# Performance work log

Measured on AMD Instinct MI355X. Metric: run time of the kernel, lower is better.

Reference implementation:

```python
import jax, jax.numpy as jnp
import numpy as np

NUM_HEADS = 8
DIM_HEAD = 64
GROUPS = 32
EPS = 1e-5


def setup_inputs() -> dict:
    key = jax.random.key(0)
    k1, k2, k3 = jax.random.split(key, 3)
    C = 512
    inner = NUM_HEADS * DIM_HEAD  # 512
    x = jax.random.normal(k1, (8, C, 32, 32), dtype=jnp.float32)
    gamma = jnp.ones((C,), dtype=jnp.float32)
    beta = jnp.zeros((C,), dtype=jnp.float32)
    w_qkv = jax.random.normal(k2, (3 * inner, C), dtype=jnp.float32) * 0.02
    w_out = jax.random.normal(k3, (C, inner), dtype=jnp.float32) * 0.02
    return {"x": x, "gamma": gamma, "beta": beta, "w_qkv": w_qkv, "w_out": w_out}


def group_norm(x, gamma, beta):
    b, c, h, w = x.shape
    xg = x.reshape(b, GROUPS, c // GROUPS, h, w)
    mean = jnp.mean(xg, axis=(2, 3, 4), keepdims=True)
    var = jnp.var(xg, axis=(2, 3, 4), keepdims=True)
    xn = ((xg - mean) * jax.lax.rsqrt(var + EPS)).reshape(b, c, h, w)
    return xn * gamma[None, :, None, None] + beta[None, :, None, None]


def reference(x, gamma, beta, w_qkv, w_out):
    b, c, h, w = x.shape
    H, d = NUM_HEADS, DIM_HEAD
    inner = H * d
    scale = d ** (-0.5)
    residual = x
    xn = group_norm(x, gamma, beta)
    # 1x1 conv (no bias) == channel matmul
    qkv = jnp.einsum('bchw,oc->bohw', xn, w_qkv)  # [b, 3*inner, h, w]
    q, k, v = jnp.split(qkv, 3, axis=1)
    def to_heads(t):
        # b (H d) h w -> b H (h w) d
        return t.reshape(b, H, d, h * w).transpose(0, 1, 3, 2)
    q, k, v = to_heads(q), to_heads(k), to_heads(v)
    attn = jnp.einsum('bhid,bhjd->bhij', q, k) * scale  # [b,H,hw,hw]
    attn = jax.nn.softmax(attn, axis=-1)
    out = jnp.einsum('bhij,bhjd->bhid', attn, v)  # [b,H,hw,d]
    # b H (h w) d -> b (H d) h w
    out = out.transpose(0, 1, 3, 2).reshape(b, inner, h, w)
    out = jnp.einsum('bchw,oc->bohw', out, w_out)
    return out + residual
```

## Files before the change

kernel.cpp:

```cpp
#include <hip/hip_runtime.h>


typedef __attribute__((ext_vector_type(8))) short bf16x8;
typedef __attribute__((ext_vector_type(4))) short bf16x4;
typedef __attribute__((ext_vector_type(4))) float f32x4;

#define NB 8
#define NC 512
#define HW 1024
#define NHEAD 8
#define DHEAD 64
#define GROUPS 32
#define CPG 16
#define QKV_N 1536

#define GLL16(gaddr, ldsaddr)                                                  \
    __builtin_amdgcn_global_load_lds(                                          \
        (const __attribute__((address_space(1))) unsigned*)(gaddr),            \
        (__attribute__((address_space(3))) unsigned*)(ldsaddr), 16, 0, 0)

__device__ alignas(64) short g_xn[(size_t)8192 * 512];
__device__ alignas(64) short g_qkv[(size_t)8192 * 1536];
__device__ alignas(64) short g_vt[(size_t)64 * 64 * 1024];
__device__ alignas(64) short g_attno[(size_t)8192 * 512];
__device__ alignas(64) short g_wqkv[(size_t)1536 * 512];
__device__ alignas(64) short g_wout[(size_t)512 * 512];

__device__ __forceinline__ float b2f(short h) {
    union { unsigned u; float f; } v;
    v.u = ((unsigned)(unsigned short)h) << 16;
    return v.f;
}
__device__ __forceinline__ short f2b(float f) {
    union { float f; unsigned u; } v;
    v.f = f;
    unsigned r = v.u + 0x7fff + ((v.u >> 16) & 1);
    return (short)(r >> 16);
}

__global__ __launch_bounds__(256) void prep_kernel(
    const float* __restrict__ x, const float* __restrict__ gamma,
    const float* __restrict__ beta, const float* __restrict__ wqkv,
    const float* __restrict__ wout) {
    int tid = threadIdx.x;
    if (blockIdx.x >= 256) {
        int wb = blockIdx.x - 256;
        for (int i = wb * 256 + tid; i < 1536 * 512; i += 64 * 256) {
            float v = wqkv[i];
            if (i < 512 * 512) v *= 0.18033688011112042f;
            g_wqkv[i] = f2b(v);
        }
        for (int i = wb * 256 + tid; i < 512 * 512; i += 64 * 256)
            g_wout[i] = f2b(wout[i]);
        return;
    }
    int b = blockIdx.x >> 5, g = blockIdx.x & 31;
    __shared__ alignas(16) short tile[CPG][HW];
    __shared__ float red[2][4];
    __shared__ float sg[CPG], sb[CPG];
    if (tid < CPG) {
        int cg = g * CPG + tid;
        sg[tid] = gamma[cg];
        sb[tid] = beta[cg];
    }
    const float* xb = x + (size_t)b * NC * HW + (size_t)g * CPG * HW;
    float s1 = 0.f, s2 = 0.f;
    #pragma unroll
    for (int it = 0; it < 8; it++) {
        int idx = tid + it * 256;
        f32x4 v0 = *(const f32x4*)(xb + idx * 8);
        f32x4 v1 = *(const f32x4*)(xb + idx * 8 + 4);
        bf16x8 w;
        #pragma unroll
        for (int j = 0; j < 4; j++) {
            s1 += v0[j] + v1[j]; s2 += v0[j] * v0[j] + v1[j] * v1[j];
            w[j] = f2b(v0[j]); w[j + 4] = f2b(v1[j]);
        }
        *(bf16x8*)(&((short*)tile)[idx * 8]) = w;
    }
    #pragma unroll
    for (int off = 32; off; off >>= 1) { s1 += __shfl_xor(s1, off); s2 += __shfl_xor(s2, off); }
    int wid = tid >> 6;
    if ((tid & 63) == 0) { red[0][wid] = s1; red[1][wid] = s2; }
    __syncthreads();
    float t1 = red[0][0] + red[0][1] + red[0][2] + red[0][3];
    float t2 = red[1][0] + red[1][1] + red[1][2] + red[1][3];
    float mean = t1 * (1.f / 16384.f);
    float var  = t2 * (1.f / 16384.f) - mean * mean;
    float inv  = rsqrtf(var + 1e-5f);
    #pragma unroll
    for (int p = 0; p < 4; p++) {
        int s = tid * 4 + p;
        bf16x8 pk0, pk1;
        #pragma unroll
        for (int cc = 0; cc < 8; cc++) {
            pk0[cc] = f2b((b2f(tile[cc][s])     - mean) * inv * sg[cc]     + sb[cc]);
            pk1[cc] = f2b((b2f(tile[cc + 8][s]) - mean) * inv * sg[cc + 8] + sb[cc + 8]);
        }
        size_t dst = ((size_t)(b * HW + s)) * NC + g * CPG;
        *(bf16x8*)(g_xn + dst)     = pk0;
        *(bf16x8*)(g_xn + dst + 8) = pk1;
    }
}

__global__ __launch_bounds__(256) void gemm_qkv() {
    const int K = NC;
    int tid = threadIdx.x, lane = tid & 63, wid = tid >> 6;
    int quad = lane >> 4, l15 = lane & 15;
    int row0 = blockIdx.x * 128;
    int col0 = blockIdx.y * 128;
    __shared__ alignas(16) short sa[128 * 64];
    __shared__ alignas(16) short sbuf[128 * 64];
    int r_lo = lane >> 3;
    int s_log = (lane & 7) ^ r_lo;
    int swz = l15 & 7;
    const short* ga = g_xn   + (size_t)(row0 + wid * 32 + r_lo) * K + s_log * 8;
    const short* gb = g_wqkv + (size_t)(col0 + wid * 32 + r_lo) * K + s_log * 8;
    int mw = (wid >> 1) * 64, nw = (wid & 1) * 64;
    f32x4 acc[4][4] = {};
    for (int k = 0; k < K; k += 64) {
        #pragma unroll
        for (int c = 0; c < 4; c++) {
            GLL16(ga + (size_t)(c * 8) * K + k, &sa[(wid * 32 + c * 8) * 64]);
            GLL16(gb + (size_t)(c * 8) * K + k, &sbuf[(wid * 32 + c * 8) * 64]);
        }
        __syncthreads();
        bf16x8 af0[4], af1[4], bf0[4], bf1[4];
        #pragma unroll
        for (int m = 0; m < 4; m++) {
            int row = mw + m * 16 + l15;
            af0[m] = *(const bf16x8*)&sa[row * 64 + ((quad ^ swz) * 8)];
            af1[m] = *(const bf16x8*)&sa[row * 64 + (((4 + quad) ^ swz) * 8)];
        }
        #pragma unroll
        for (int n = 0; n < 4; n++) {
            int row = nw + n * 16 + l15;
            bf0[n] = *(const bf16x8*)&sbuf[row * 64 + ((quad ^ swz) * 8)];
            bf1[n] = *(const bf16x8*)&sbuf[row * 64 + (((4 + quad) ^ swz) * 8)];
        }
        #pragma unroll
        for (int m = 0; m < 4; m++)
            #pragma unroll
            for (int n = 0; n < 4; n++) {
                acc[m][n] = __builtin_amdgcn_mfma_f32_16x16x32_bf16(af0[m], bf0[n], acc[m][n], 0, 0, 0);
                acc[m][n] = __builtin_amdgcn_mfma_f32_16x16x32_bf16(af1[m], bf1[n], acc[m][n], 0, 0, 0);
            }
        __syncthreads();
    }
    #pragma unroll
    for (int m = 0; m < 4; m++)
        #pragma unroll
        for (int n = 0; n < 4; n++)
            #pragma unroll
            for (int r = 0; r < 4; r++) {
                int row = row0 + mw + m * 16 + quad * 4 + r;
                int col = col0 + nw + n * 16 + l15;
                g_qkv[(size_t)row * QKV_N + col] = f2b(acc[m][n][r]);
            }
}

__global__ __launch_bounds__(256) void transpose_v() {
    int bh = blockIdx.x & 63, st = blockIdx.x >> 6;
    int b = bh >> 3, h = bh & 7;
    int tid = threadIdx.x;
    __shared__ alignas(16) short tile[64][72];
    int s0 = st * 64;
    #pragma unroll
    for (int cc = 0; cc < 2; cc++) {
        int idx = tid + cc * 256;
        int s = idx >> 3, dc = idx & 7;
        *(bf16x8*)&tile[s][dc * 8] =
            *(const bf16x8*)(g_qkv + ((size_t)(b * HW + s0 + s)) * QKV_N + 1024 + h * DHEAD + dc * 8);
    }
    __syncthreads();
    #pragma unroll
    for (int cc = 0; cc < 2; cc++) {
        int idx = tid + cc * 256;
        int d = idx & 63, sc = idx >> 6;
        bf16x8 o;
        #pragma unroll
        for (int j = 0; j < 8; j++) o[j] = tile[sc * 8 + j][d];
        *(bf16x8*)(g_vt + ((size_t)(bh * 64 + d)) * HW + s0 + sc * 8) = o;
    }
}

__global__ __launch_bounds__(256) void attn_kernel() {
    int bh = blockIdx.x & 63, qt = blockIdx.x >> 6;
    int b = bh >> 3, h = bh & 7;
    int tid = threadIdx.x, lane = tid & 63, wid = tid >> 6;
    int quad = lane >> 4, l15 = lane & 15;
    __shared__ alignas(16) short kt[2][64 * 64];
    __shared__ alignas(16) short vt[2][64 * 64];
    __shared__ alignas(16) short pt4[4][16][16][4];
    int qrow0 = qt * 64 + wid * 16;

    const short* qb = g_qkv + ((size_t)(b * HW + qrow0 + l15)) * QKV_N + h * DHEAD + quad * 8;
    bf16x8 aq0 = *(const bf16x8*)qb;
    bf16x8 aq1 = *(const bf16x8*)(qb + 32);
    f32x4 acc_o[4] = {};
    f32x4 acc_l = {};
    bf16x8 vone;
    #pragma unroll
    for (int j = 0; j < 8; j++) vone[j] = (short)0x3f80;

    int r_lo = lane >> 3;
    int s_log = (lane & 7) ^ r_lo;
    int swz = l15 & 7;

    auto stage = [&](int it, int bufi) {
        int t0 = it * 64;
        #pragma unroll
        for (int c = 0; c < 2; c++) {
            int r = wid * 16 + c * 8 + r_lo;
            GLL16(g_qkv + ((size_t)(b * HW + t0 + r)) * QKV_N + 512 + h * DHEAD + s_log * 8,
                  &kt[bufi][(wid * 16 + c * 8) * 64]);
            GLL16(g_vt + ((size_t)(bh * 64 + r)) * HW + t0 + s_log * 8,
                  &vt[bufi][(wid * 16 + c * 8) * 64]);
        }
    };

    stage(0, 0);
    __syncthreads();
    for (int it = 0; it < 16; it++) {
        int cur = it & 1;
        if (it < 15) stage(it + 1, cur ^ 1);
        #pragma unroll
        for (int sub = 0; sub < 4; sub++) {
            int row = sub * 16 + l15;
            bf16x8 k0 = *(const bf16x8*)&kt[cur][row * 64 + ((quad ^ swz) * 8)];
            bf16x8 k1 = *(const bf16x8*)&kt[cur][row * 64 + (((4 + quad) ^ swz) * 8)];
            f32x4 z = {};
            z = __builtin_amdgcn_mfma_f32_16x16x32_bf16(k0, aq0, z, 0, 0, 0);
            z = __builtin_amdgcn_mfma_f32_16x16x32_bf16(k1, aq1, z, 0, 0, 0);
            float e0, e1, e2, e3;
            asm("v_exp_f32 %0, %1" : "=v"(e0) : "v"(z[0]));
            asm("v_exp_f32 %0, %1" : "=v"(e1) : "v"(z[1]));
            asm("v_exp_f32 %0, %1" : "=v"(e2) : "v"(z[2]));
            asm("v_exp_f32 %0, %1" : "=v"(e3) : "v"(z[3]));
            union { unsigned w[2]; bf16x4 s; } pk;
            asm("v_cvt_pk_bf16_f32 %0, %1, %2" : "=v"(pk.w[0]) : "v"(e0), "v"(e1));
            asm("v_cvt_pk_bf16_f32 %0, %1, %2" : "=v"(pk.w[1]) : "v"(e2), "v"(e3));
            *(bf16x4*)&pt4[wid][sub * 4 + quad][l15][0] = pk.s;
        }
        asm volatile("" ::: "memory");
        bf16x8 ap0, ap1;
        {
            union { bf16x4 hh[2]; bf16x8 v; } cc;
            cc.hh[0] = *(const bf16x4*)&pt4[wid][quad * 2][l15][0];
            cc.hh[1] = *(const bf16x4*)&pt4[wid][quad * 2 + 1][l15][0];
            ap0 = cc.v;
            cc.hh[0] = *(const bf16x4*)&pt4[wid][8 + quad * 2][l15][0];
            cc.hh[1] = *(const bf16x4*)&pt4[wid][8 + quad * 2 + 1][l15][0];
            ap1 = cc.v;
        }
        acc_l = __builtin_amdgcn_mfma_f32_16x16x32_bf16(ap0, vone, acc_l, 0, 0, 0);
        acc_l = __builtin_amdgcn_mfma_f32_16x16x32_bf16(ap1, vone, acc_l, 0, 0, 0);
        #pragma unroll
        for (int nd = 0; nd < 4; nd++) {
            int row = nd * 16 + l15;
            bf16x8 bv0 = *(const bf16x8*)&vt[cur][row * 64 + ((quad ^ swz) * 8)];
            bf16x8 bv1 = *(const bf16x8*)&vt[cur][row * 64 + (((4 + quad) ^ swz) * 8)];
            acc_o[nd] = __builtin_amdgcn_mfma_f32_16x16x32_bf16(ap0, bv0, acc_o[nd], 0, 0, 0);
            acc_o[nd] = __builtin_amdgcn_mfma_f32_16x16x32_bf16(ap1, bv1, acc_o[nd], 0, 0, 0);
        }
        __syncthreads();
    }
    #pragma unroll
    for (int r = 0; r < 4; r++) {
        float invl = 1.f / acc_l[r];
        size_t row = (size_t)(b * HW + qrow0 + quad * 4 + r);
        #pragma unroll
        for (int nd = 0; nd < 4; nd++)
            g_attno[row * NC + h * DHEAD + nd * 16 + l15] = f2b(acc_o[nd][r] * invl);
    }
}

__global__ __launch_bounds__(256) void gemm_out(
    const float* __restrict__ xres, float* __restrict__ out) {
    const int K = NC;
    int tid = threadIdx.x, lane = tid & 63, wid = tid >> 6;
    int quad = lane >> 4, l15 = lane & 15;
    int row0 = blockIdx.x * 128;
    int col0 = blockIdx.y * 128;
    __shared__ alignas(16) short sa[128 * 32];
    __shared__ alignas(16) short sbuf[128 * 32];
    int srow = wid * 32 + (lane >> 2);
    int scol = (lane & 3) * 8;
    const short* ga = g_wout  + (size_t)(row0 + srow) * K + scol;
    const short* gb = g_attno + (size_t)(col0 + srow) * K + scol;
    short* la = sa   + wid * 1024;
    short* lb = sbuf + wid * 1024;
    int mw = (wid >> 1) * 64, nw = (wid & 1) * 64;
    f32x4 acc[4][4] = {};
    for (int k = 0; k < K; k += 32) {
        GLL16(ga + k, la);
        GLL16(ga + (size_t)16 * K + k, la + 512);
        GLL16(gb + k, lb);
        GLL16(gb + (size_t)16 * K + k, lb + 512);
        __syncthreads();
        bf16x8 af[4], bfv[4];
        #pragma unroll
        for (int m = 0; m < 4; m++) af[m]  = *(const bf16x8*)&sa[(mw + m * 16 + l15) * 32 + quad * 8];
        #pragma unroll
        for (int n = 0; n < 4; n++) bfv[n] = *(const bf16x8*)&sbuf[(nw + n * 16 + l15) * 32 + quad * 8];
        #pragma unroll
        for (int m = 0; m < 4; m++)
            #pragma unroll
            for (int n = 0; n < 4; n++)
                acc[m][n] = __builtin_amdgcn_mfma_f32_16x16x32_bf16(af[m], bfv[n], acc[m][n], 0, 0, 0);
        __syncthreads();
    }
    #pragma unroll
    for (int m = 0; m < 4; m++)
        #pragma unroll
        for (int n = 0; n < 4; n++)
            #pragma unroll
            for (int r = 0; r < 4; r++) {
                int o  = row0 + mw + m * 16 + quad * 4 + r;
                int bs = col0 + nw + n * 16 + l15;
                size_t addr = (size_t)(bs >> 10) * ((size_t)NC * HW) + (size_t)o * HW + (bs & 1023);
                out[addr] = acc[m][n][r] + xres[addr];
            }
}

extern "C" void kernel_launch(void* const* d_in, const int* in_sizes, int n_in,
                              void* d_out, int out_size, void* d_ws, size_t ws_size,
                              hipStream_t stream) {
    const float* x     = (const float*)d_in[0];
    const float* gamma = (const float*)d_in[1];
    const float* beta  = (const float*)d_in[2];
    const float* wqkv  = (const float*)d_in[3];
    const float* wout  = (const float*)d_in[4];
    float* out = (float*)d_out;

    prep_kernel<<<dim3(320), dim3(256), 0, stream>>>(x, gamma, beta, wqkv, wout);
    gemm_qkv<<<dim3(64, 12), dim3(256), 0, stream>>>();
    transpose_v<<<dim3(1024), dim3(256), 0, stream>>>();
    attn_kernel<<<dim3(1024), dim3(256), 0, stream>>>();
    gemm_out<<<dim3(4, 64), dim3(256), 0, stream>>>(x, out);
}
```

Measured before the change: 156.0 us.

## Switch attention to 32x32x16 MFMA with register-level P transpose via permlane32 swap

Rewrites the attention kernel to use 32x32x16 bf16 MFMAs, with each wave handling 32 query rows, so each block covers 128 query rows and the grid is halved. The exponentiated scores are repacked in registers with v_permlane32_swap instead of round-tripping through LDS, which removes the per-iteration P staging buffer and its LDS traffic. This doubles K/V tile reuse per block load, at the cost of more accumulator registers and fewer blocks in flight.

```diff
diff --git a/kernel.cpp b/kernel.cpp
--- a/kernel.cpp
+++ b/kernel.cpp
@@ -4,6 +4,7 @@
 typedef __attribute__((ext_vector_type(8))) short bf16x8;
 typedef __attribute__((ext_vector_type(4))) short bf16x4;
 typedef __attribute__((ext_vector_type(4))) float f32x4;
+typedef __attribute__((ext_vector_type(16))) float f32x16;
 
 #define NB 8
 #define NC 512
@@ -188,24 +189,23 @@
     int bh = blockIdx.x & 63, qt = blockIdx.x >> 6;
     int b = bh >> 3, h = bh & 7;
     int tid = threadIdx.x, lane = tid & 63, wid = tid >> 6;
-    int quad = lane >> 4, l15 = lane & 15;
+    int l31 = lane & 31, hl = lane >> 5;
     __shared__ alignas(16) short kt[2][64 * 64];
     __shared__ alignas(16) short vt[2][64 * 64];
-    __shared__ alignas(16) short pt4[4][16][16][4];
-    int qrow0 = qt * 64 + wid * 16;
-
-    const short* qb = g_qkv + ((size_t)(b * HW + qrow0 + l15)) * QKV_N + h * DHEAD + quad * 8;
-    bf16x8 aq0 = *(const bf16x8*)qb;
-    bf16x8 aq1 = *(const bf16x8*)(qb + 32);
-    f32x4 acc_o[4] = {};
-    f32x4 acc_l = {};
+    int qrow0 = qt * 128 + wid * 32;
+
+    const short* qb = g_qkv + ((size_t)(b * HW + qrow0 + l31)) * QKV_N + h * DHEAD + hl * 8;
+    bf16x8 aq[4];
+    #pragma unroll
+    for (int ks = 0; ks < 4; ks++) aq[ks] = *(const bf16x8*)(qb + ks * 16);
+
+    f32x16 acc_o0 = {}, acc_o1 = {}, acc_l = {};
     bf16x8 vone;
     #pragma unroll
     for (int j = 0; j < 8; j++) vone[j] = (short)0x3f80;
 
     int r_lo = lane >> 3;
     int s_log = (lane & 7) ^ r_lo;
-    int swz = l15 & 7;
 
     auto stage = [&](int it, int bufi) {
         int t0 = it * 64;
@@ -224,54 +224,66 @@
     for (int it = 0; it < 16; it++) {
         int cur = it & 1;
         if (it < 15) stage(it + 1, cur ^ 1);
-        #pragma unroll
-        for (int sub = 0; sub < 4; sub++) {
-            int row = sub * 16 + l15;
-            bf16x8 k0 = *(const bf16x8*)&kt[cur][row * 64 + ((quad ^ swz) * 8)];
-            bf16x8 k1 = *(const bf16x8*)&kt[cur][row * 64 + (((4 + quad) ^ swz) * 8)];
-            f32x4 z = {};
-            z = __builtin_amdgcn_mfma_f32_16x16x32_bf16(k0, aq0, z, 0, 0, 0);
-            z = __builtin_amdgcn_mfma_f32_16x16x32_bf16(k1, aq1, z, 0, 0, 0);
+        f32x16 z0 = {}, z1 = {};
+        #pragma unroll
+        for (int ks = 0; ks < 4; ks++) {
+            int g0 = ks * 2 + hl;
+            int rowa = l31;
+            bf16x8 k0 = *(const bf16x8*)&kt[cur][rowa * 64 + ((g0 ^ (rowa & 7)) * 8)];
+            z0 = __builtin_amdgcn_mfma_f32_32x32x16_bf16(k0, aq[ks], z0, 0, 0, 0);
+            int rowb = 32 + l31;
+            bf16x8 k1 = *(const bf16x8*)&kt[cur][rowb * 64 + ((g0 ^ (rowb & 7)) * 8)];
+            z1 = __builtin_amdgcn_mfma_f32_32x32x16_bf16(k1, aq[ks], z1, 0, 0, 0);
+        }
+        unsigned u0[8], u1[8];
+        #pragma unroll
+        for (int p = 0; p < 8; p++) {
             float e0, e1, e2, e3;
-            asm("v_exp_f32 %0, %1" : "=v"(e0) : "v"(z[0]));
-            asm("v_exp_f32 %0, %1" : "=v"(e1) : "v"(z[1]));
-            asm("v_exp_f32 %0, %1" : "=v"(e2) : "v"(z[2]));
-            asm("v_exp_f32 %0, %1" : "=v"(e3) : "v"(z[3]));
-            union { unsigned w[2]; bf16x4 s; } pk;
-            asm("v_cvt_pk_bf16_f32 %0, %1, %2" : "=v"(pk.w[0]) : "v"(e0), "v"(e1));
-            asm("v_cvt_pk_bf16_f32 %0, %1, %2" : "=v"(pk.w[1]) : "v"(e2), "v"(e3));
-            *(bf16x4*)&pt4[wid][sub * 4 + quad][l15][0] = pk.s;
-        }
-        asm volatile("" ::: "memory");
-        bf16x8 ap0, ap1;
-        {
-            union { bf16x4 hh[2]; bf16x8 v; } cc;
-            cc.hh[0] = *(const bf16x4*)&pt4[wid][quad * 2][l15][0];
-            cc.hh[1] = *(const bf16x4*)&pt4[wid][quad * 2 + 1][l15][0];
-            ap0 = cc.v;
-            cc.hh[0] = *(const bf16x4*)&pt4[wid][8 + quad * 2][l15][0];
-            cc.hh[1] = *(const bf16x4*)&pt4[wid][8 + quad * 2 + 1][l15][0];
-            ap1 = cc.v;
-        }
-        acc_l = __builtin_amdgcn_mfma_f32_16x16x32_bf16(ap0, vone, acc_l, 0, 0, 0);
-        acc_l = __builtin_amdgcn_mfma_f32_16x16x32_bf16(ap1, vone, acc_l, 0, 0, 0);
-        #pragma unroll
-        for (int nd = 0; nd < 4; nd++) {
-            int row = nd * 16 + l15;
-            bf16x8 bv0 = *(const bf16x8*)&vt[cur][row * 64 + ((quad ^ swz) * 8)];
-            bf16x8 bv1 = *(const bf16x8*)&vt[cur][row * 64 + (((4 + quad) ^ swz) * 8)];
-            acc_o[nd] = __builtin_amdgcn_mfma_f32_16x16x32_bf16(ap0, bv0, acc_o[nd], 0, 0, 0);
-            acc_o[nd] = __builtin_amdgcn_mfma_f32_16x16x32_bf16(ap1, bv1, acc_o[nd], 0, 0, 0);
-        }
-        __syncthreads();
-    }
-    #pragma unroll
-    for (int r = 0; r < 4; r++) {
+            asm("v_exp_f32 %0, %1" : "=v"(e0) : "v"(z0[2 * p]));
+            asm("v_exp_f32 %0, %1" : "=v"(e1) : "v"(z0[2 * p + 1]));
+            asm("v_exp_f32 %0, %1" : "=v"(e2) : "v"(z1[2 * p]));
+            asm("v_exp_f32 %0, %1" : "=v"(e3) : "v"(z1[2 * p + 1]));
+            asm("v_cvt_pk_bf16_f32 %0, %1, %2" : "=v"(u0[p]) : "v"(e0), "v"(e1));
+            asm("v_cvt_pk_bf16_f32 %0, %1, %2" : "=v"(u1[p]) : "v"(e2), "v"(e3));
+        }
+        bf16x8 ap[4];
+        #pragma unroll
+        for (int th = 0; th < 2; th++) {
+            #pragma unroll
+            for (int ks1 = 0; ks1 < 2; ks1++) {
+                unsigned x0 = th ? u1[4 * ks1]     : u0[4 * ks1];
+                unsigned y0 = th ? u1[4 * ks1 + 2] : u0[4 * ks1 + 2];
+                unsigned x1 = th ? u1[4 * ks1 + 1] : u0[4 * ks1 + 1];
+                unsigned y1 = th ? u1[4 * ks1 + 3] : u0[4 * ks1 + 3];
+                asm("v_permlane32_swap_b32 %0, %1" : "+v"(x0), "+v"(y0));
+                asm("v_permlane32_swap_b32 %0, %1" : "+v"(x1), "+v"(y1));
+                union { unsigned w[4]; bf16x8 v; } pa;
+                pa.w[0] = x0; pa.w[1] = x1; pa.w[2] = y0; pa.w[3] = y1;
+                ap[th * 2 + ks1] = pa.v;
+            }
+        }
+        #pragma unroll
+        for (int ks = 0; ks < 4; ks++)
+            acc_l = __builtin_amdgcn_mfma_f32_32x32x16_bf16(ap[ks], vone, acc_l, 0, 0, 0);
+        #pragma unroll
+        for (int ks = 0; ks < 4; ks++) {
+            int gt = ks * 2 + hl;
+            int rowd0 = l31;
+            bf16x8 bv0 = *(const bf16x8*)&vt[cur][rowd0 * 64 + ((gt ^ (rowd0 & 7)) * 8)];
+            acc_o0 = __builtin_amdgcn_mfma_f32_32x32x16_bf16(ap[ks], bv0, acc_o0, 0, 0, 0);
+            int rowd1 = 32 + l31;
+            bf16x8 bv1 = *(const bf16x8*)&vt[cur][rowd1 * 64 + ((gt ^ (rowd1 & 7)) * 8)];
+            acc_o1 = __builtin_amdgcn_mfma_f32_32x32x16_bf16(ap[ks], bv1, acc_o1, 0, 0, 0);
+        }
+        __syncthreads();
+    }
+    #pragma unroll
+    for (int r = 0; r < 16; r++) {
+        int m = (r & 3) + 8 * (r >> 2) + 4 * hl;
         float invl = 1.f / acc_l[r];
-        size_t row = (size_t)(b * HW + qrow0 + quad * 4 + r);
-        #pragma unroll
-        for (int nd = 0; nd < 4; nd++)
-            g_attno[row * NC + h * DHEAD + nd * 16 + l15] = f2b(acc_o[nd][r] * invl);
+        size_t row = (size_t)(b * HW + qrow0 + m);
+        g_attno[row * NC + h * DHEAD + l31]      = f2b(acc_o0[r] * invl);
+        g_attno[row * NC + h * DHEAD + 32 + l31] = f2b(acc_o1[r] * invl);
     }
 }
 
@@ -336,6 +348,6 @@
     prep_kernel<<<dim3(320), dim3(256), 0, stream>>>(x, gamma, beta, wqkv, wout);
     gemm_qkv<<<dim3(64, 12), dim3(256), 0, stream>>>();
     transpose_v<<<dim3(1024), dim3(256), 0, stream>>>();
-    attn_kernel<<<dim3(1024), dim3(256), 0, stream>>>();
+    attn_kernel<<<dim3(512), dim3(256), 0, stream>>>();
     gemm_out<<<dim3(4, 64), dim3(256), 0, stream>>>(x, out);
 }
```

Result: no change. 154.9 us (-0.7%).
